# Kernel optimization log

Hardware: AMD Instinct MI355X
Metric: run time of the kernel (lower is better)

The kernel has to match this reference:

```python
import jax, jax.numpy as jnp
import numpy as np

KH, KW = 7, 7            # extraction kernel
EH, EW = 5, 5            # effective (cropped) kernel
PAD = (KH - EH) // 2     # = 1
EPS = 1e-7


def _extract_patches(x):
    # x: [B,H,W,C] -> patches [B,Ho,Wo,KH,KW,C], stride 1, VALID padding
    B, H, Wd, C = x.shape
    Ho, Wo = H - KH + 1, Wd - KW + 1
    rows = []
    for i in range(KH):
        cols = [x[:, i:i + Ho, j:j + Wo, :] for j in range(KW)]
        rows.append(jnp.stack(cols, axis=3))          # [B,Ho,Wo,KW,C]
    return jnp.stack(rows, axis=3)                     # [B,Ho,Wo,KH,KW,C]


def _rotate_bilinear(patches, angles):
    # patches: [N,KH,KW,C]; angles: [N]. Mirrors tf.contrib.image
    # angles_to_projective_transforms + transform(BILINEAR, fill=0).
    # Note: the layer's det(matrix)==0 NEAREST fallback never fires (det==1).
    N = patches.shape[0]
    c, s = jnp.cos(angles), jnp.sin(angles)
    Wm1, Hm1 = jnp.float32(KW - 1), jnp.float32(KH - 1)
    xo = (Wm1 - (c * Wm1 - s * Hm1)) * 0.5
    yo = (Hm1 - (s * Wm1 + c * Hm1)) * 0.5
    scale = jnp.float32(1.0 + EPS)   # transforms /= transforms[:,8:9]+1e-7
    a0, a1, a2 = c / scale, -s / scale, xo / scale
    a3, a4, a5 = s / scale, c / scale, yo / scale
    yg, xg = jnp.meshgrid(jnp.arange(KH, dtype=jnp.float32),
                          jnp.arange(KW, dtype=jnp.float32), indexing='ij')
    x_in = a0[:, None, None] * xg + a1[:, None, None] * yg + a2[:, None, None]
    y_in = a3[:, None, None] * xg + a4[:, None, None] * yg + a5[:, None, None]
    x0f = jnp.floor(x_in); y0f = jnp.floor(y_in)
    wx1 = x_in - x0f; wx0 = 1.0 - wx1
    wy1 = y_in - y0f; wy0 = 1.0 - wy1
    x0 = x0f.astype(jnp.int32); x1 = x0 + 1
    y0 = y0f.astype(jnp.int32); y1 = y0 + 1
    nidx = jnp.arange(N)[:, None, None]

    def corner(yi, xi, w):
        valid = ((xi >= 0) & (xi < KW) & (yi >= 0) & (yi < KH)).astype(patches.dtype)
        v = patches[nidx, jnp.clip(yi, 0, KH - 1), jnp.clip(xi, 0, KW - 1)]
        return (w * valid)[..., None] * v

    return (corner(y0, x0, wy0 * wx0) + corner(y0, x1, wy0 * wx1) +
            corner(y1, x0, wy1 * wx0) + corner(y1, x1, wy1 * wx1))


def reference(x, W, b):
    B, H, Wd, C = x.shape
    patches = _extract_patches(x)                      # [B,Ho,Wo,KH,KW,C]
    _, Ho, Wo = patches.shape[:3]
    intensity = jnp.sum(patches, axis=-1)              # [B,Ho,Wo,KH,KW]
    row_idx = jnp.repeat(jnp.arange(KH, dtype=jnp.float32), KW)   # rowMulti
    col_idx = jnp.tile(jnp.arange(KW, dtype=jnp.float32), KH)     # colMulti
    flat = intensity.reshape(-1, KH * KW)              # [N, KH*KW]
    denom = jnp.sum(flat, -1) + EPS
    cr = jnp.sum(flat * row_idx, -1) / denom - (KH - 1) / 2.0
    cc = jnp.sum(flat * col_idx, -1) / denom - (KW - 1) / 2.0
    angle = jnp.arctan2(cr, cc + EPS)                  # [N]
    patches_n = patches.reshape(-1, KH, KW, C)         # [N,KH,KW,C]
    rot = _rotate_bilinear(patches_n, angle)
    rot = rot[:, PAD:PAD + EH, PAD:PAD + EW, :]        # crop to effective
    rot = rot.reshape(B, Ho, Wo, EH * EW * C)
    w_flat = W.reshape(W.shape[0], -1)                 # [F, EH*EW*C]
    out = jnp.einsum('bhwk,fk->bhwf', rot, w_flat) + b
    return out


def setup_inputs() -> dict:
    key = jax.random.key(0)
    kx, kw, _ = jax.random.split(key, 3)
    x = jax.random.normal(kx, (8, 64, 64, 32), dtype=jnp.float32)
    W = jax.random.normal(kw, (64, EH, EW, 32), dtype=jnp.float32) * 0.05
    b = jnp.zeros((64,), dtype=jnp.float32)
    return {"x": x, "W": W, "b": b}
```

## Files before the change

kernel.cpp:

```cpp
#include <hip/hip_runtime.h>
#include <hip/hip_bf16.h>

#define EPSF 1e-7f
#define B_ 8
#define H_ 64
#define W_ 64
#define C_ 32
#define HO 58
#define WO 58
#define NF 64
#define KDIM 800

#define XBS 40

typedef __bf16 v8bf __attribute__((ext_vector_type(8)));
typedef float  v4f  __attribute__((ext_vector_type(4)));
typedef float  v2f  __attribute__((ext_vector_type(2)));

__global__ void k_wpack(const float* __restrict__ W, __bf16* __restrict__ Wp) {
    int t = blockIdx.x*256 + threadIdx.x;
    int j = t & 7; int lane = (t >> 3) & 63; int rest = t >> 9;
    int kb = rest % 25; int nt = rest / 25;
    int f = nt*16 + (lane & 15);
    int k = kb*32 + (lane >> 4)*8 + j;
    Wp[t] = (__bf16)W[f*KDIM + k];
}

__global__ __launch_bounds__(256, 3)
void k_main(const float* __restrict__ x, const v8bf* __restrict__ Wp,
            const float* __restrict__ bias, float* __restrict__ out) {
    __shared__ __bf16 xtb[10][22][XBS];
    __shared__ float  Srow[10][22];
    __shared__ float4 pars[64];

    int tid = threadIdx.x;
    int wv = tid >> 6, lane = tid & 63;
    int m = lane & 15, q = lane >> 4;

    int L = blockIdx.x + 4*(blockIdx.y + 15*blockIdx.z);
    int newL = (L & 7)*60 + (L >> 3);
    int b   = newL / 60;
    int rem = newL - b*60;
    int rg  = rem >> 2;
    int cg  = rem & 3;
    int ho0 = rg*4, wo0 = cg*16;
    int npx = WO - wo0; if (npx > 16) npx = 16;

    if (tid < 220) {
        int r = tid / 22, c = tid - r*22;
        int xr = ho0 + r; if (xr > H_-1) xr = H_-1;
        int xc = wo0 + c; if (xc > W_-1) xc = W_-1;
        const float* src = x + (size_t)((b*H_ + xr)*W_ + xc)*C_;
        float4 vq[8];
#pragma unroll
        for (int qq = 0; qq < 8; qq++) vq[qq] = *(const float4*)(src + qq*4);
        float s = 0.f;
#pragma unroll
        for (int qq = 0; qq < 8; qq++) s += vq[qq].x + vq[qq].y + vq[qq].z + vq[qq].w;
        Srow[r][c] = s;
#pragma unroll
        for (int h8 = 0; h8 < 4; h8++) {
            v8bf o;
            o[0]=(__bf16)vq[h8*2].x;   o[1]=(__bf16)vq[h8*2].y;
            o[2]=(__bf16)vq[h8*2].z;   o[3]=(__bf16)vq[h8*2].w;
            o[4]=(__bf16)vq[h8*2+1].x; o[5]=(__bf16)vq[h8*2+1].y;
            o[6]=(__bf16)vq[h8*2+1].z; o[7]=(__bf16)vq[h8*2+1].w;
            *(v8bf*)&xtb[r][c][h8*8] = o;
        }
    }
    __syncthreads();

    if (tid < 64) {
        int r0 = tid >> 4, c0 = tid & 15;
        float den = 0.f, crn = 0.f, ccn = 0.f;
#pragma unroll
        for (int i = 0; i < 7; i++)
#pragma unroll
            for (int j = 0; j < 7; j++) {
                float v = Srow[r0 + i][c0 + j];
                den += v; crn += v*(float)i; ccn += v*(float)j;
            }
        float dt = den + EPSF;
        float cr = crn/dt - 3.0f;
        float cx = ccn/dt - 3.0f + EPSF;
        float r2 = cr*cr + cx*cx;
        float inv = r2 > 0.f ? rsqrtf(r2) : 0.f;
        float c_ = r2 > 0.f ? cx*inv : 1.0f;
        float s_ = cr*inv;
        const float scale = 1.0f + EPSF;
        float pc  = c_/scale, ps = s_/scale;
        float pxo = (6.0f - (c_*6.0f - s_*6.0f))*0.5f/scale;
        float pyo = (6.0f - (s_*6.0f + c_*6.0f))*0.5f/scale;
        pars[tid] = make_float4(pc, ps, pxo, pyo);
    }
    __syncthreads();

    float4 pp = pars[(wv << 4) | m];
    float pc = pp.x, ps = pp.y, pxo = pp.z, pyo = pp.w;

    float bv[4];
#pragma unroll
    for (int nt = 0; nt < 4; nt++) bv[nt] = bias[nt*16 + m];

    const v8bf* wp = Wp + lane;
    const __bf16* patch = &xtb[wv][m][q*8];

    v4f acc0 = {0.f,0.f,0.f,0.f}, acc1 = {0.f,0.f,0.f,0.f};
    v4f acc2 = {0.f,0.f,0.f,0.f}, acc3 = {0.f,0.f,0.f,0.f};

#pragma unroll 1
    for (int py = 0; py < 5; py++) {
        float yy = (float)(py + 1);
#pragma unroll
        for (int pxx = 0; pxx < 5; pxx++) {
            int kb = py*5 + pxx;
            float xx = (float)(pxx + 1);

            v8bf wf0 = wp[(0*25 + kb)*64];
            v8bf wf1 = wp[(1*25 + kb)*64];
            v8bf wf2 = wp[(2*25 + kb)*64];
            v8bf wf3 = wp[(3*25 + kb)*64];

            float xin = pc*xx - ps*yy + pxo;
            float yin = ps*xx + pc*yy + pyo;
            float x0f = floorf(xin), y0f = floorf(yin);
            float wx1 = xin - x0f, wx0 = 1.0f - wx1;
            float wy1 = yin - y0f, wy0 = 1.0f - wy1;
            int ix0 = (int)x0f, iy0 = (int)y0f;
            int ix1 = ix0 + 1,  iy1 = iy0 + 1;

            v2f a8[4];
#pragma unroll
            for (int d = 0; d < 4; d++) a8[d] = (v2f){0.f, 0.f};

            auto corner = [&](int yi, int xi, float wgt) {
                bool valid = (xi >= 0) & (xi < 7) & (yi >= 0) & (yi < 7);
                int cy  = yi < 0 ? 0 : (yi > 6 ? 6 : yi);
                int cx2 = xi < 0 ? 0 : (xi > 6 ? 6 : xi);
                float wq = valid ? wgt : 0.0f;
                union { v8bf v; unsigned u[4]; } uv;
                uv.v = *(const v8bf*)(patch + (cy*22 + cx2)*XBS);
                v2f w2 = (v2f){wq, wq};
#pragma unroll
                for (int d = 0; d < 4; d++) {
                    v2f val = (v2f){ __uint_as_float(uv.u[d] << 16),
                                     __uint_as_float(uv.u[d] & 0xffff0000u) };
                    a8[d] += w2 * val;
                }
            };
            corner(iy0, ix0, wy0*wx0);
            corner(iy0, ix1, wy0*wx1);
            corner(iy1, ix0, wy1*wx0);
            corner(iy1, ix1, wy1*wx1);

            v8bf af;
#pragma unroll
            for (int d = 0; d < 4; d++) {
                af[2*d]   = (__bf16)a8[d].x;
                af[2*d+1] = (__bf16)a8[d].y;
            }
            acc0 = __builtin_amdgcn_mfma_f32_16x16x32_bf16(af, wf0, acc0, 0, 0, 0);
            acc1 = __builtin_amdgcn_mfma_f32_16x16x32_bf16(af, wf1, acc1, 0, 0, 0);
            acc2 = __builtin_amdgcn_mfma_f32_16x16x32_bf16(af, wf2, acc2, 0, 0, 0);
            acc3 = __builtin_amdgcn_mfma_f32_16x16x32_bf16(af, wf3, acc3, 0, 0, 0);
        }
    }

    int ho = ho0 + wv;
    if (ho < HO) {
        size_t rowbase = (size_t)(b*HO + ho)*WO + wo0;
#pragma unroll
        for (int r = 0; r < 4; r++) {
            int px = q*4 + r;
            if (px < npx) {
                float* op = out + (rowbase + px)*NF + m;
                op[0]  = acc0[r] + bv[0];
                op[16] = acc1[r] + bv[1];
                op[32] = acc2[r] + bv[2];
                op[48] = acc3[r] + bv[3];
            }
        }
    }
}

extern "C" void kernel_launch(void* const* d_in, const int* in_sizes, int n_in,
                              void* d_out, int out_size, void* d_ws, size_t ws_size,
                              hipStream_t stream) {
    const float* x    = (const float*)d_in[0];
    const float* W    = (const float*)d_in[1];
    const float* bias = (const float*)d_in[2];
    float* out = (float*)d_out;
    __bf16* Wp = (__bf16*)d_ws;

    k_wpack<<<dim3(200), 256, 0, stream>>>(W, Wp);
    k_main<<<dim3(4, 15, 8), 256, 0, stream>>>(x, (const v8bf*)Wp, bias, out);
}
```

Measured before the change: 79.57 us.

## Split K across wave pairs with LDS reduction and double-buffer weight loads

Each block now covers 2 output rows instead of 4. Two waves per row each process about half of the 25 kernel-position K blocks, and the partial accumulators are summed through shared memory before the store. Weight fragments are double-buffered so the next global load is issued ahead of the current interpolation and MFMA work. The grid doubles and launch bounds ask for 4 blocks per SM to raise parallelism and hide latency, at the cost of an extra barrier, the LDS reduction, and duplicate halo loads across blocks.

```diff
diff --git a/kernel.cpp b/kernel.cpp
--- a/kernel.cpp
+++ b/kernel.cpp
@@ -26,31 +26,32 @@
     Wp[t] = (__bf16)W[f*KDIM + k];
 }
 
-__global__ __launch_bounds__(256, 3)
+__global__ __launch_bounds__(256, 4)
 void k_main(const float* __restrict__ x, const v8bf* __restrict__ Wp,
             const float* __restrict__ bias, float* __restrict__ out) {
-    __shared__ __bf16 xtb[10][22][XBS];
-    __shared__ float  Srow[10][22];
-    __shared__ float4 pars[64];
+    __shared__ __bf16 xtb[8][22][XBS];
+    __shared__ float  Srow[8][22];
+    __shared__ float4 pars[32];
+    __shared__ float  redu[2][64][20];
 
     int tid = threadIdx.x;
     int wv = tid >> 6, lane = tid & 63;
     int m = lane & 15, q = lane >> 4;
-
-    int L = blockIdx.x + 4*(blockIdx.y + 15*blockIdx.z);
-    int newL = (L & 7)*60 + (L >> 3);
-    int b   = newL / 60;
-    int rem = newL - b*60;
+    int rh = wv & 1, kh = wv >> 1;
+
+    int L = blockIdx.x + 4*(blockIdx.y + 29*blockIdx.z);
+    int newL = (L & 7)*116 + (L >> 3);
+    int b   = newL / 116;
+    int rem = newL - b*116;
     int rg  = rem >> 2;
     int cg  = rem & 3;
-    int ho0 = rg*4, wo0 = cg*16;
+    int ho0 = rg*2, wo0 = cg*16;
     int npx = WO - wo0; if (npx > 16) npx = 16;
 
-    if (tid < 220) {
+    if (tid < 176) {
         int r = tid / 22, c = tid - r*22;
-        int xr = ho0 + r; if (xr > H_-1) xr = H_-1;
         int xc = wo0 + c; if (xc > W_-1) xc = W_-1;
-        const float* src = x + (size_t)((b*H_ + xr)*W_ + xc)*C_;
+        const float* src = x + (size_t)((b*H_ + ho0 + r)*W_ + xc)*C_;
         float4 vq[8];
 #pragma unroll
         for (int qq = 0; qq < 8; qq++) vq[qq] = *(const float4*)(src + qq*4);
@@ -70,7 +71,7 @@
     }
     __syncthreads();
 
-    if (tid < 64) {
+    if (tid < 32) {
         int r0 = tid >> 4, c0 = tid & 15;
         float den = 0.f, crn = 0.f, ccn = 0.f;
 #pragma unroll
@@ -95,89 +96,117 @@
     }
     __syncthreads();
 
-    float4 pp = pars[(wv << 4) | m];
+    float4 pp = pars[(rh << 4) | m];
     float pc = pp.x, ps = pp.y, pxo = pp.z, pyo = pp.w;
 
-    float bv[4];
-#pragma unroll
-    for (int nt = 0; nt < 4; nt++) bv[nt] = bias[nt*16 + m];
-
     const v8bf* wp = Wp + lane;
-    const __bf16* patch = &xtb[wv][m][q*8];
+    const __bf16* patch = &xtb[rh][m][q*8];
 
     v4f acc0 = {0.f,0.f,0.f,0.f}, acc1 = {0.f,0.f,0.f,0.f};
     v4f acc2 = {0.f,0.f,0.f,0.f}, acc3 = {0.f,0.f,0.f,0.f};
 
+    int kb0 = kh*13;
+    int nkb = 13 - kh;
+    int kblast = kb0 + nkb - 1;
+
+    auto loadw = [&](v8bf* dst, int kbi) {
+        dst[0] = wp[(0*25 + kbi)*64];
+        dst[1] = wp[(1*25 + kbi)*64];
+        dst[2] = wp[(2*25 + kbi)*64];
+        dst[3] = wp[(3*25 + kbi)*64];
+    };
+
+    auto body = [&](int kb, const v8bf* wf) {
+        unsigned ukb = (unsigned)kb;
+        int py = (int)(ukb/5u);
+        int pxx = kb - py*5;
+        float yy = (float)(py + 1);
+        float xx = (float)(pxx + 1);
+
+        float xin = pc*xx - ps*yy + pxo;
+        float yin = ps*xx + pc*yy + pyo;
+        float x0f = floorf(xin), y0f = floorf(yin);
+        float wx1 = xin - x0f, wx0 = 1.0f - wx1;
+        float wy1 = yin - y0f, wy0 = 1.0f - wy1;
+        int ix0 = (int)x0f, iy0 = (int)y0f;
+        int ix1 = ix0 + 1,  iy1 = iy0 + 1;
+
+        v2f a8[4];
+#pragma unroll
+        for (int d = 0; d < 4; d++) a8[d] = (v2f){0.f, 0.f};
+
+        auto corner = [&](int yi, int xi, float wgt) {
+            bool valid = (xi >= 0) & (xi < 7) & (yi >= 0) & (yi < 7);
+            int cy  = yi < 0 ? 0 : (yi > 6 ? 6 : yi);
+            int cx2 = xi < 0 ? 0 : (xi > 6 ? 6 : xi);
+            float wq = valid ? wgt : 0.0f;
+            union { v8bf v; unsigned u[4]; } uv;
+            uv.v = *(const v8bf*)(patch + (cy*22 + cx2)*XBS);
+            v2f w2 = (v2f){wq, wq};
+#pragma unroll
+            for (int d = 0; d < 4; d++) {
+                v2f val = (v2f){ __uint_as_float(uv.u[d] << 16),
+                                 __uint_as_float(uv.u[d] & 0xffff0000u) };
+                a8[d] += w2 * val;
+            }
+        };
+        corner(iy0, ix0, wy0*wx0);
+        corner(iy0, ix1, wy0*wx1);
+        corner(iy1, ix0, wy1*wx0);
+        corner(iy1, ix1, wy1*wx1);
+
+        v8bf af;
+#pragma unroll
+        for (int d = 0; d < 4; d++) {
+            af[2*d]   = (__bf16)a8[d].x;
+            af[2*d+1] = (__bf16)a8[d].y;
+        }
+        acc0 = __builtin_amdgcn_mfma_f32_16x16x32_bf16(af, wf[0], acc0, 0, 0, 0);
+        acc1 = __builtin_amdgcn_mfma_f32_16x16x32_bf16(af, wf[1], acc1, 0, 0, 0);
+        acc2 = __builtin_amdgcn_mfma_f32_16x16x32_bf16(af, wf[2], acc2, 0, 0, 0);
+        acc3 = __builtin_amdgcn_mfma_f32_16x16x32_bf16(af, wf[3], acc3, 0, 0, 0);
+    };
+
+    v8bf wfA[4], wfB[4];
+    loadw(wfA, kb0);
+    int i = 0;
 #pragma unroll 1
-    for (int py = 0; py < 5; py++) {
-        float yy = (float)(py + 1);
-#pragma unroll
-        for (int pxx = 0; pxx < 5; pxx++) {
-            int kb = py*5 + pxx;
-            float xx = (float)(pxx + 1);
-
-            v8bf wf0 = wp[(0*25 + kb)*64];
-            v8bf wf1 = wp[(1*25 + kb)*64];
-            v8bf wf2 = wp[(2*25 + kb)*64];
-            v8bf wf3 = wp[(3*25 + kb)*64];
-
-            float xin = pc*xx - ps*yy + pxo;
-            float yin = ps*xx + pc*yy + pyo;
-            float x0f = floorf(xin), y0f = floorf(yin);
-            float wx1 = xin - x0f, wx0 = 1.0f - wx1;
-            float wy1 = yin - y0f, wy0 = 1.0f - wy1;
-            int ix0 = (int)x0f, iy0 = (int)y0f;
-            int ix1 = ix0 + 1,  iy1 = iy0 + 1;
-
-            v2f a8[4];
-#pragma unroll
-            for (int d = 0; d < 4; d++) a8[d] = (v2f){0.f, 0.f};
-
-            auto corner = [&](int yi, int xi, float wgt) {
-                bool valid = (xi >= 0) & (xi < 7) & (yi >= 0) & (yi < 7);
-                int cy  = yi < 0 ? 0 : (yi > 6 ? 6 : yi);
-                int cx2 = xi < 0 ? 0 : (xi > 6 ? 6 : xi);
-                float wq = valid ? wgt : 0.0f;
-                union { v8bf v; unsigned u[4]; } uv;
-                uv.v = *(const v8bf*)(patch + (cy*22 + cx2)*XBS);
-                v2f w2 = (v2f){wq, wq};
-#pragma unroll
-                for (int d = 0; d < 4; d++) {
-                    v2f val = (v2f){ __uint_as_float(uv.u[d] << 16),
-                                     __uint_as_float(uv.u[d] & 0xffff0000u) };
-                    a8[d] += w2 * val;
-                }
-            };
-            corner(iy0, ix0, wy0*wx0);
-            corner(iy0, ix1, wy0*wx1);
-            corner(iy1, ix0, wy1*wx0);
-            corner(iy1, ix1, wy1*wx1);
-
-            v8bf af;
-#pragma unroll
-            for (int d = 0; d < 4; d++) {
-                af[2*d]   = (__bf16)a8[d].x;
-                af[2*d+1] = (__bf16)a8[d].y;
-            }
-            acc0 = __builtin_amdgcn_mfma_f32_16x16x32_bf16(af, wf0, acc0, 0, 0, 0);
-            acc1 = __builtin_amdgcn_mfma_f32_16x16x32_bf16(af, wf1, acc1, 0, 0, 0);
-            acc2 = __builtin_amdgcn_mfma_f32_16x16x32_bf16(af, wf2, acc2, 0, 0, 0);
-            acc3 = __builtin_amdgcn_mfma_f32_16x16x32_bf16(af, wf3, acc3, 0, 0, 0);
-        }
-    }
-
-    int ho = ho0 + wv;
-    if (ho < HO) {
+    for (; i + 2 <= nkb; i += 2) {
+        loadw(wfB, kb0 + i + 1);
+        body(kb0 + i, wfA);
+        int nx = kb0 + i + 2; if (nx > kblast) nx = kblast;
+        loadw(wfA, nx);
+        body(kb0 + i + 1, wfB);
+    }
+    if (i < nkb) body(kblast, wfA);
+
+    if (kh == 1) {
+        *(v4f*)&redu[rh][lane][0]  = acc0;
+        *(v4f*)&redu[rh][lane][4]  = acc1;
+        *(v4f*)&redu[rh][lane][8]  = acc2;
+        *(v4f*)&redu[rh][lane][12] = acc3;
+    }
+    __syncthreads();
+    if (kh == 0) {
+        acc0 += *(const v4f*)&redu[rh][lane][0];
+        acc1 += *(const v4f*)&redu[rh][lane][4];
+        acc2 += *(const v4f*)&redu[rh][lane][8];
+        acc3 += *(const v4f*)&redu[rh][lane][12];
+
+        float bv0 = bias[m], bv1 = bias[16 + m];
+        float bv2 = bias[32 + m], bv3 = bias[48 + m];
+
+        int ho = ho0 + rh;
         size_t rowbase = (size_t)(b*HO + ho)*WO + wo0;
 #pragma unroll
         for (int r = 0; r < 4; r++) {
             int px = q*4 + r;
             if (px < npx) {
                 float* op = out + (rowbase + px)*NF + m;
-                op[0]  = acc0[r] + bv[0];
-                op[16] = acc1[r] + bv[1];
-                op[32] = acc2[r] + bv[2];
-                op[48] = acc3[r] + bv[3];
+                op[0]  = acc0[r] + bv0;
+                op[16] = acc1[r] + bv1;
+                op[32] = acc2[r] + bv2;
+                op[48] = acc3[r] + bv3;
             }
         }
     }
@@ -193,5 +222,5 @@
     __bf16* Wp = (__bf16*)d_ws;
 
     k_wpack<<<dim3(200), 256, 0, stream>>>(W, Wp);
-    k_main<<<dim3(4, 15, 8), 256, 0, stream>>>(x, (const v8bf*)Wp, bias, out);
+    k_main<<<dim3(4, 29, B_), 256, 0, stream>>>(x, (const v8bf*)Wp, bias, out);
 }
```

After: 76.83 us. 3.4% less time.
